# Optimization experiments

Measured on AMD Instinct MI355X. Metric: run time of the kernel, lower is better.

## Reference

```python
import jax, jax.numpy as jnp
import numpy as np

B, N, D, H = 4, 8192, 1024, 16
C = D // H  # head dim = 64
EPS = 1e-6


def setup_inputs() -> dict:
    key = jax.random.key(0)
    ks = jax.random.split(key, 8)
    sc = 0.02
    return {
        "q": jax.random.normal(ks[0], (B, N, D), jnp.float32),
        "k": jax.random.normal(ks[1], (B, N, D), jnp.float32),
        "v": jax.random.normal(ks[2], (B, N, D), jnp.float32),
        "Wq": jax.random.normal(ks[3], (D, D), jnp.float32) * sc,
        "Wk": jax.random.normal(ks[4], (D, D), jnp.float32) * sc,
        "Wv": jax.random.normal(ks[5], (D, D), jnp.float32) * sc,
        "Wproj": jax.random.normal(ks[6], (D, D), jnp.float32) * sc,
        "focusing_factor": jnp.asarray(3.0, jnp.float32),
    }


def _to_heads(x):
    # b n (h c) -> (b h) n c
    return x.reshape(B, N, H, C).transpose(0, 2, 1, 3).reshape(B * H, N, C)


def reference(q, k, v, Wq, Wk, Wv, Wproj, focusing_factor):
    # projections (torch Linear: x @ W.T, no bias)
    qp = q @ Wq.T
    kp = k @ Wk.T
    vp = v @ Wv.T

    def feature_map(x):
        # |GELU(x)| + eps, then focused renormalization:
        # softmax(focusing_factor * log(f)) * mean(f)
        f = jnp.abs(jax.nn.gelu(x, approximate=False)) + EPS
        f_norm = f.mean(axis=-1, keepdims=True)
        return jax.nn.softmax(jnp.log(f) * focusing_factor, axis=-1) * f_norm

    qf = feature_map(qp)
    kf = feature_map(kp)

    qh = _to_heads(qf)  # [B*H, N, C]
    kh = _to_heads(kf)
    vh = _to_heads(vp)

    k_mean = kh.mean(axis=1)  # [B*H, C]
    z_inv = jnp.einsum('bnd,bd->bn', qh, k_mean) + EPS  # [B*H, N]

    # (k/sqrt(N))^T (v/sqrt(N)) == (k^T v)/N
    kv = jnp.einsum('bnc,bnd->bcd', kh, vh) / N  # [B*H, C, C]
    y = jnp.einsum('bic,bcd->bid', qh, kv) / z_inv[..., None]  # [B*H, N, C]

    y = y.reshape(B, H, N, C).transpose(0, 2, 1, 3).reshape(B, N, D)
    return y @ Wproj.T
```

## Files before the change

### kernel.cpp

```cpp
#include <hip/hip_runtime.h>

using f16 = _Float16;
typedef __attribute__((ext_vector_type(4))) _Float16 f16x4;
typedef __attribute__((ext_vector_type(8))) _Float16 f16x8;
typedef __attribute__((ext_vector_type(4))) float f32x4;

#define DEVI __device__ __forceinline__

namespace {

constexpr int BB = 4;
constexpr int NN = 8192;
constexpr int DD = 1024;
constexpr int MTOT = BB * NN;
constexpr float FSCALE = 64.0f;
constexpr float ZCONST = 64.0f * 64.0f * (8192.0f * 1e-6f);

DEVI void gl16(const void* g, void* l) {
  __builtin_amdgcn_global_load_lds(
      (__attribute__((address_space(1))) void*)(void*)g,
      (__attribute__((address_space(3))) void*)l, 16, 0, 0);
}

DEVI float wsum(float v) {
#pragma unroll
  for (int m = 32; m > 0; m >>= 1) v += __shfl_xor(v, m, 64);
  return v;
}
DEVI float wmaxr(float v) {
#pragma unroll
  for (int m = 32; m > 0; m >>= 1) v = fmaxf(v, __shfl_xor(v, m, 64));
  return v;
}
DEVI float block_sum(float v, float* sred, int tid) {
  v = wsum(v);
  __syncthreads();
  if ((tid & 63) == 0) sred[tid >> 6] = v;
  __syncthreads();
  return sred[0] + sred[1] + sred[2] + sred[3];
}
DEVI float block_max(float v, float* sred, int tid) {
  v = wmaxr(v);
  __syncthreads();
  if ((tid & 63) == 0) sred[tid >> 6] = v;
  __syncthreads();
  return fmaxf(fmaxf(sred[0], sred[1]), fmaxf(sred[2], sred[3]));
}

struct CastArgs {
  const float* src[8];
  f16* dst[8];
  int n4[8];
};

__global__ __launch_bounds__(256) void cast_kernel(CastArgs a) {
  const int z = blockIdx.y;
  const float4* __restrict__ s = (const float4*)a.src[z];
  f16x4* __restrict__ d = (f16x4*)a.dst[z];
  const int n4 = a.n4[z];
  for (int i = blockIdx.x * blockDim.x + threadIdx.x; i < n4;
       i += gridDim.x * blockDim.x) {
    float4 f = s[i];
    f16x4 o = {(f16)f.x, (f16)f.y, (f16)f.z, (f16)f.w};
    d[i] = o;
  }
}

struct Gemm3 {
  const f16* A[3];
  const f16* Bt[3];
  void* C[3];
};
struct Gemm3f {
  const float* A[3];
  const f16* Bt[3];
  f16* C[3];
};

#define GEMM_PREAMBLE()                                                      \
  constexpr int K = DD;                                                      \
  constexpr int N = DD;                                                      \
  constexpr int NKT = K / 64;                                                \
  const int nx = gridDim.x;                                                  \
  int lin = blockIdx.y * nx + blockIdx.x;                                    \
  const int cpx = (gridDim.y * nx) >> 3;                                     \
  lin = (lin & 7) * cpx + (lin >> 3);                                        \
  const size_t row0 = (size_t)(lin / nx) * 256;                              \
  const size_t col0 = (size_t)(lin % nx) * 256;                              \
  const int tid = threadIdx.x, lane = tid & 63, wv = tid >> 6;               \
  const int wm = wv >> 2, wn = wv & 3;                                       \
  const int fr = lane & 15, f7 = lane & 7, kq = lane >> 4;                   \
  const int srow = wv * 8 + (lane >> 3);                                     \
  const int ssw = (lane & 7) ^ ((lane >> 3) & 7);                            \
  const int c0e = (kq ^ f7) * 8;

__global__ __launch_bounds__(512, 2) void gemm256_fa(Gemm3f P) {
  GEMM_PREAMBLE()
  const int z = blockIdx.z;
  const float* __restrict__ A = P.A[z];
  const f16* __restrict__ Bt = P.Bt[z];
  f16* __restrict__ C = P.C[z];

  __shared__ __align__(16) f16 LA[2][2][8192];
  __shared__ __align__(16) f16 LB[2][2][8192];

  auto stageB = [&](int kts, int half) {
    const f16* src = Bt + (col0 + half * 128 + srow) * K + kts * 64 + ssw * 8;
    f16* dst = &LB[kts & 1][half][wv * 512];
#pragma unroll
    for (int c = 0; c < 2; ++c) gl16(src + (size_t)c * 64 * K, dst + c * 4096);
  };

  const int ar = tid >> 2;
  const int ac2 = (tid & 3) * 2;
  auto loadA = [&](int kts, float4* r) {
#pragma unroll
    for (int half = 0; half < 2; ++half) {
      const float* src = A + (row0 + half * 128 + ar) * (size_t)K + kts * 64;
#pragma unroll
      for (int c = 0; c < 2; ++c) {
        r[half * 4 + 2 * c + 0] = *(const float4*)(src + (ac2 + c) * 8);
        r[half * 4 + 2 * c + 1] = *(const float4*)(src + (ac2 + c) * 8 + 4);
      }
    }
  };
  auto writeA = [&](int kts, const float4* r) {
#pragma unroll
    for (int half = 0; half < 2; ++half) {
      f16* base = &LA[kts & 1][half][ar * 64];
#pragma unroll
      for (int c = 0; c < 2; ++c) {
        const float4 lo = r[half * 4 + 2 * c], hi = r[half * 4 + 2 * c + 1];
        f16x8 o = {(f16)lo.x, (f16)lo.y, (f16)lo.z, (f16)lo.w,
                   (f16)hi.x, (f16)hi.y, (f16)hi.z, (f16)hi.w};
        *(f16x8*)&base[((ac2 + c) ^ (ar & 7)) * 8] = o;
      }
    }
  };

  f32x4 acc[8][4];
#pragma unroll
  for (int i = 0; i < 8; ++i)
#pragma unroll
    for (int j = 0; j < 4; ++j) acc[i][j] = f32x4{0.f, 0.f, 0.f, 0.f};

  float4 ra[8];
  loadA(0, ra);
  stageB(0, 0); stageB(0, 1);
  asm volatile("s_waitcnt vmcnt(0)" ::: "memory");
  writeA(0, ra);
  asm volatile("s_waitcnt lgkmcnt(0)" ::: "memory");
  loadA(1, ra);
  __builtin_amdgcn_s_barrier();

  for (int kt = 0; kt < NKT; ++kt) {
    const int buf = kt & 1;
    const f16* Ah = LA[buf][wm];
    const f16* Bh = &LB[buf][wn >> 1][(wn & 1) * 4096];
    f16x8 a0[8], a1[8], b0[4], b1[4];

#pragma unroll
    for (int mi = 0; mi < 8; ++mi)
      a0[mi] = *(const f16x8*)&Ah[(mi * 16 + fr) * 64 + c0e];
#pragma unroll
    for (int ni = 0; ni < 4; ++ni)
      b0[ni] = *(const f16x8*)&Bh[(ni * 16 + fr) * 64 + c0e];
    if (kt + 1 < NKT) stageB(kt + 1, 0);
    __builtin_amdgcn_s_barrier();
    asm volatile("s_waitcnt lgkmcnt(0)" ::: "memory");
    __builtin_amdgcn_sched_barrier(0);
    __builtin_amdgcn_s_setprio(1);
#pragma unroll
    for (int mi = 0; mi < 4; ++mi)
#pragma unroll
      for (int ni = 0; ni < 4; ++ni)
        acc[mi][ni] = __builtin_amdgcn_mfma_f32_16x16x32_f16(
            a0[mi], b0[ni], acc[mi][ni], 0, 0, 0);
    __builtin_amdgcn_s_setprio(0);
    __builtin_amdgcn_s_barrier();

#pragma unroll
    for (int mi = 0; mi < 8; ++mi)
      a1[mi] = *(const f16x8*)&Ah[(mi * 16 + fr) * 64 + (c0e ^ 32)];
    if (kt + 1 < NKT) stageB(kt + 1, 1);
    __builtin_amdgcn_s_barrier();
    asm volatile("s_waitcnt lgkmcnt(0)" ::: "memory");
    __builtin_amdgcn_sched_barrier(0);
    __builtin_amdgcn_s_setprio(1);
#pragma unroll
    for (int mi = 4; mi < 8; ++mi)
#pragma unroll
      for (int ni = 0; ni < 4; ++ni)
        acc[mi][ni] = __builtin_amdgcn_mfma_f32_16x16x32_f16(
            a0[mi], b0[ni], acc[mi][ni], 0, 0, 0);
    __builtin_amdgcn_s_setprio(0);
    __builtin_amdgcn_s_barrier();

#pragma unroll
    for (int ni = 0; ni < 4; ++ni)
      b1[ni] = *(const f16x8*)&Bh[(ni * 16 + fr) * 64 + (c0e ^ 32)];
    __builtin_amdgcn_s_barrier();
    asm volatile("s_waitcnt lgkmcnt(0)" ::: "memory");
    __builtin_amdgcn_sched_barrier(0);
    __builtin_amdgcn_s_setprio(1);
#pragma unroll
    for (int mi = 0; mi < 4; ++mi)
#pragma unroll
      for (int ni = 0; ni < 4; ++ni)
        acc[mi][ni] = __builtin_amdgcn_mfma_f32_16x16x32_f16(
            a1[mi], b1[ni], acc[mi][ni], 0, 0, 0);
    __builtin_amdgcn_s_setprio(0);
    __builtin_amdgcn_s_barrier();

    __builtin_amdgcn_s_setprio(1);
#pragma unroll
    for (int mi = 4; mi < 8; ++mi)
#pragma unroll
      for (int ni = 0; ni < 4; ++ni)
        acc[mi][ni] = __builtin_amdgcn_mfma_f32_16x16x32_f16(
            a1[mi], b1[ni], acc[mi][ni], 0, 0, 0);
    __builtin_amdgcn_s_setprio(0);
    asm volatile("s_waitcnt vmcnt(0)" ::: "memory");
    __builtin_amdgcn_sched_barrier(0);
    if (kt + 1 < NKT) {
      writeA(kt + 1, ra);
      asm volatile("s_waitcnt lgkmcnt(0)" ::: "memory");
      if (kt + 2 < NKT) loadA(kt + 2, ra);
    }
    __builtin_amdgcn_s_barrier();
  }

#pragma unroll
  for (int mi = 0; mi < 8; ++mi)
#pragma unroll
    for (int ni = 0; ni < 4; ++ni) {
      const size_t colv = col0 + wn * 64 + ni * 16 + fr;
#pragma unroll
      for (int r = 0; r < 4; ++r) {
        const size_t rowv = row0 + wm * 128 + mi * 16 + (lane >> 4) * 4 + r;
        C[rowv * N + colv] = (f16)acc[mi][ni][r];
      }
    }
}

template <typename OutT>
__global__ __launch_bounds__(512, 2) void gemm256(Gemm3 P) {
  GEMM_PREAMBLE()
  const int z = blockIdx.z;
  const f16* __restrict__ A = P.A[z];
  const f16* __restrict__ Bt = P.Bt[z];
  OutT* __restrict__ C = (OutT*)P.C[z];

  __shared__ __align__(16) f16 LA[2][2][8192];
  __shared__ __align__(16) f16 LB[2][2][8192];

  auto stageA = [&](int kts, int half) {
    const f16* src = A + (row0 + half * 128 + srow) * K + kts * 64 + ssw * 8;
    f16* dst = &LA[kts & 1][half][wv * 512];
#pragma unroll
    for (int c = 0; c < 2; ++c) gl16(src + (size_t)c * 64 * K, dst + c * 4096);
  };
  auto stageB = [&](int kts, int half) {
    const f16* src = Bt + (col0 + half * 128 + srow) * K + kts * 64 + ssw * 8;
    f16* dst = &LB[kts & 1][half][wv * 512];
#pragma unroll
    for (int c = 0; c < 2; ++c) gl16(src + (size_t)c * 64 * K, dst + c * 4096);
  };

  f32x4 acc[8][4];
#pragma unroll
  for (int i = 0; i < 8; ++i)
#pragma unroll
    for (int j = 0; j < 4; ++j) acc[i][j] = f32x4{0.f, 0.f, 0.f, 0.f};

  stageA(0, 0); stageA(0, 1); stageB(0, 0); stageB(0, 1);
  stageA(1, 0); stageA(1, 1);
  asm volatile("s_waitcnt vmcnt(4)" ::: "memory");
  __builtin_amdgcn_s_barrier();

  for (int kt = 0; kt < NKT; ++kt) {
    const int buf = kt & 1;
    const f16* Ah = LA[buf][wm];
    const f16* Bh = &LB[buf][wn >> 1][(wn & 1) * 4096];
    f16x8 a0[8], a1[8], b0[4], b1[4];

#pragma unroll
    for (int mi = 0; mi < 8; ++mi)
      a0[mi] = *(const f16x8*)&Ah[(mi * 16 + fr) * 64 + c0e];
#pragma unroll
    for (int ni = 0; ni < 4; ++ni)
      b0[ni] = *(const f16x8*)&Bh[(ni * 16 + fr) * 64 + c0e];
    if (kt < NKT - 1) stageB(kt + 1, 0);
    __builtin_amdgcn_s_barrier();
    asm volatile("s_waitcnt lgkmcnt(0)" ::: "memory");
    __builtin_amdgcn_sched_barrier(0);
    __builtin_amdgcn_s_setprio(1);
#pragma unroll
    for (int mi = 0; mi < 4; ++mi)
#pragma unroll
      for (int ni = 0; ni < 4; ++ni)
        acc[mi][ni] = __builtin_amdgcn_mfma_f32_16x16x32_f16(
            a0[mi], b0[ni], acc[mi][ni], 0, 0, 0);
    __builtin_amdgcn_s_setprio(0);
    __builtin_amdgcn_s_barrier();

#pragma unroll
    for (int mi = 0; mi < 8; ++mi)
      a1[mi] = *(const f16x8*)&Ah[(mi * 16 + fr) * 64 + (c0e ^ 32)];
    if (kt < NKT - 1) stageB(kt + 1, 1);
    __builtin_amdgcn_s_barrier();
    asm volatile("s_waitcnt lgkmcnt(0)" ::: "memory");
    __builtin_amdgcn_sched_barrier(0);
    __builtin_amdgcn_s_setprio(1);
#pragma unroll
    for (int mi = 4; mi < 8; ++mi)
#pragma unroll
      for (int ni = 0; ni < 4; ++ni)
        acc[mi][ni] = __builtin_amdgcn_mfma_f32_16x16x32_f16(
            a0[mi], b0[ni], acc[mi][ni], 0, 0, 0);
    __builtin_amdgcn_s_setprio(0);
    __builtin_amdgcn_s_barrier();

#pragma unroll
    for (int ni = 0; ni < 4; ++ni)
      b1[ni] = *(const f16x8*)&Bh[(ni * 16 + fr) * 64 + (c0e ^ 32)];
    if (kt < NKT - 2) stageA(kt + 2, 0);
    __builtin_amdgcn_s_barrier();
    asm volatile("s_waitcnt lgkmcnt(0)" ::: "memory");
    __builtin_amdgcn_sched_barrier(0);
    __builtin_amdgcn_s_setprio(1);
#pragma unroll
    for (int mi = 0; mi < 4; ++mi)
#pragma unroll
      for (int ni = 0; ni < 4; ++ni)
        acc[mi][ni] = __builtin_amdgcn_mfma_f32_16x16x32_f16(
            a1[mi], b1[ni], acc[mi][ni], 0, 0, 0);
    __builtin_amdgcn_s_setprio(0);
    __builtin_amdgcn_s_barrier();

    if (kt < NKT - 2) stageA(kt + 2, 1);
    __builtin_amdgcn_s_barrier();
    __builtin_amdgcn_s_setprio(1);
#pragma unroll
    for (int mi = 4; mi < 8; ++mi)
#pragma unroll
      for (int ni = 0; ni < 4; ++ni)
        acc[mi][ni] = __builtin_amdgcn_mfma_f32_16x16x32_f16(
            a1[mi], b1[ni], acc[mi][ni], 0, 0, 0);
    __builtin_amdgcn_s_setprio(0);
    if (kt < NKT - 2)
      asm volatile("s_waitcnt vmcnt(4)" ::: "memory");
    else
      asm volatile("s_waitcnt vmcnt(0)" ::: "memory");
    __builtin_amdgcn_s_barrier();
  }

#pragma unroll
  for (int mi = 0; mi < 8; ++mi)
#pragma unroll
    for (int ni = 0; ni < 4; ++ni) {
      const size_t colv = col0 + wn * 64 + ni * 16 + fr;
#pragma unroll
      for (int r = 0; r < 4; ++r) {
        const size_t rowv = row0 + wm * 128 + mi * 16 + (lane >> 4) * 4 + r;
        C[rowv * N + colv] = (OutT)acc[mi][ni][r];
      }
    }
}

__global__ __launch_bounds__(256) void feature_kernel(
    const f16* __restrict__ qp, const f16* __restrict__ kp,
    f16* __restrict__ qf, f16* __restrict__ kf, const float* __restrict__ ffp) {
  const int row = blockIdx.x;
  const int tid = threadIdx.x;
  const bool isq = (blockIdx.y == 0);
  const f16* __restrict__ src = isq ? qp : kp;
  f16* __restrict__ dst = isq ? qf : kf;
  const float ff = ffp[0];
  __shared__ float sred[4];

  f16x4 xv = ((const f16x4*)src)[(size_t)row * 256 + tid];
  float f0[4];
  float ps = 0.f;
#pragma unroll
  for (int j = 0; j < 4; ++j) {
    float x = (float)xv[j];
    float g = 0.5f * x * (1.0f + erff(x * 0.70710678118654752f));
    float fv = fabsf(g) + 1e-6f;
    f0[j] = fv;
    ps += fv;
  }
  float fsum = block_sum(ps, sred, tid);
  float t[4];
  float pm = -1e30f;
#pragma unroll
  for (int j = 0; j < 4; ++j) {
    t[j] = ff * __logf(f0[j]);
    pm = fmaxf(pm, t[j]);
  }
  float tmax = block_max(pm, sred, tid);
  float e[4];
  float es = 0.f;
#pragma unroll
  for (int j = 0; j < 4; ++j) {
    e[j] = __expf(t[j] - tmax);
    es += e[j];
  }
  float esum = block_sum(es, sred, tid);
  const float scale = fsum * (1.0f / 1024.0f) / esum * FSCALE;
  f16x4 o;
#pragma unroll
  for (int j = 0; j < 4; ++j) o[j] = (f16)(e[j] * scale);
  ((f16x4*)dst)[(size_t)row * 256 + tid] = o;
}

__global__ __launch_bounds__(256) void kv_kernel(
    const f16* __restrict__ kf, const f16* __restrict__ vp,
    float* __restrict__ kvsum, float* __restrict__ colsum) {
  const int bh = blockIdx.x;
  const int b = bh >> 4, h = bh & 15;
  const int tid = threadIdx.x, lane = tid & 63, wave = tid >> 6;
  __shared__ __align__(16) f16 kt[32 * 64];
  __shared__ __align__(16) f16 vt[32 * 64];
  __shared__ float csred[4][64];

  f32x4 acc[4];
#pragma unroll
  for (int ni = 0; ni < 4; ++ni) acc[ni] = f32x4{0.f, 0.f, 0.f, 0.f};
  float cpart = 0.f;

  const int srow = wave * 8 + (lane >> 3);
  const int scol = (lane & 7) * 8;
  const int colbase = h * 64;
  const int n0base = blockIdx.y * 512;

  for (int n0 = n0base; n0 < n0base + 512; n0 += 32) {
    const size_t gofs = ((size_t)(b * NN + n0 + srow)) * DD + colbase + scol;
    gl16(kf + gofs, &kt[wave * 512]);
    gl16(vp + gofs, &vt[wave * 512]);
    __syncthreads();
    {
      const int c = tid & 63;
      const int r0 = (tid >> 6) * 8;
#pragma unroll
      for (int rr = 0; rr < 8; ++rr) cpart += (float)kt[(r0 + rr) * 64 + c];
    }
    f16x8 a, bfr[4];
#pragma unroll
    for (int j = 0; j < 8; ++j)
      a[j] = kt[((lane >> 4) * 8 + j) * 64 + wave * 16 + (lane & 15)];
#pragma unroll
    for (int ni = 0; ni < 4; ++ni)
#pragma unroll
      for (int j = 0; j < 8; ++j)
        bfr[ni][j] = vt[((lane >> 4) * 8 + j) * 64 + ni * 16 + (lane & 15)];
#pragma unroll
    for (int ni = 0; ni < 4; ++ni)
      acc[ni] = __builtin_amdgcn_mfma_f32_16x16x32_f16(a, bfr[ni], acc[ni], 0, 0, 0);
    __syncthreads();
  }
#pragma unroll
  for (int ni = 0; ni < 4; ++ni)
#pragma unroll
    for (int r = 0; r < 4; ++r) {
      const int c = wave * 16 + (lane >> 4) * 4 + r;
      const int d = ni * 16 + (lane & 15);
      atomicAdd(&kvsum[(size_t)bh * 4096 + c * 64 + d], acc[ni][r]);
    }
  csred[tid >> 6][tid & 63] = cpart;
  __syncthreads();
  if (tid < 64)
    atomicAdd(&colsum[bh * 64 + tid],
              csred[0][tid] + csred[1][tid] + csred[2][tid] + csred[3][tid]);
}

__global__ __launch_bounds__(256) void y_kernel(
    const f16* __restrict__ qf, const f16* __restrict__ kv16,
    const float* __restrict__ colsum, f16* __restrict__ y) {
  const int bh = blockIdx.x, b = bh >> 4, h = bh & 15;
  const int n0 = blockIdx.y * 128;
  const int tid = threadIdx.x, lane = tid & 63, wave = tid >> 6;
  __shared__ __align__(16) f16 qs[128 * 64];
  __shared__ __align__(16) f16 kvs[64 * 64];
  __shared__ float cs[64];
  __shared__ float zr[128];

#pragma unroll
  for (int cc = 0; cc < 4; ++cc) {
    const int r = wave * 32 + cc * 8 + (lane >> 3);
    gl16(qf + ((size_t)(b * NN + n0 + r)) * DD + h * 64 + (lane & 7) * 8,
         &qs[(wave * 4 + cc) * 512]);
  }
#pragma unroll
  for (int cc = 0; cc < 2; ++cc) {
    const int r = wave * 16 + cc * 8 + (lane >> 3);
    gl16(kv16 + (size_t)bh * 4096 + r * 64 + (lane & 7) * 8,
         &kvs[(wave * 2 + cc) * 512]);
  }
  if (tid < 64) cs[tid] = colsum[bh * 64 + tid];
  __syncthreads();
  if (tid < 128) {
    float zv = 0.f;
    for (int cc = 0; cc < 64; ++cc) {
      const int c = (cc + tid) & 63;
      zv += (float)qs[tid * 64 + c] * cs[c];
    }
    zr[tid] = zv + ZCONST;
  }
  __syncthreads();

  f32x4 acc[2][4];
#pragma unroll
  for (int mi = 0; mi < 2; ++mi)
#pragma unroll
    for (int ni = 0; ni < 4; ++ni) acc[mi][ni] = f32x4{0.f, 0.f, 0.f, 0.f};

#pragma unroll
  for (int ks = 0; ks < 2; ++ks) {
    f16x8 a[2], bfr[4];
#pragma unroll
    for (int mi = 0; mi < 2; ++mi)
      a[mi] = *(const f16x8*)&qs[(wave * 32 + mi * 16 + (lane & 15)) * 64 +
                                 ks * 32 + (lane >> 4) * 8];
#pragma unroll
    for (int ni = 0; ni < 4; ++ni)
#pragma unroll
      for (int j = 0; j < 8; ++j)
        bfr[ni][j] = kvs[(ks * 32 + (lane >> 4) * 8 + j) * 64 + ni * 16 + (lane & 15)];
#pragma unroll
    for (int mi = 0; mi < 2; ++mi)
#pragma unroll
      for (int ni = 0; ni < 4; ++ni)
        acc[mi][ni] = __builtin_amdgcn_mfma_f32_16x16x32_f16(
            a[mi], bfr[ni], acc[mi][ni], 0, 0, 0);
  }
#pragma unroll
  for (int mi = 0; mi < 2; ++mi)
#pragma unroll
    for (int ni = 0; ni < 4; ++ni)
#pragma unroll
      for (int r = 0; r < 4; ++r) {
        const int rrow = wave * 32 + mi * 16 + (lane >> 4) * 4 + r;
        const int d = ni * 16 + (lane & 15);
        const float yv = acc[mi][ni][r] / zr[rrow];
        y[((size_t)(b * NN + n0 + rrow)) * DD + h * 64 + d] = (f16)yv;
      }
}

}

extern "C" void kernel_launch(void* const* d_in, const int* in_sizes, int n_in,
                              void* d_out, int out_size, void* d_ws, size_t ws_size,
                              hipStream_t stream) {
  const float* q = (const float*)d_in[0];
  const float* k = (const float*)d_in[1];
  const float* v = (const float*)d_in[2];
  const float* Wq = (const float*)d_in[3];
  const float* Wk = (const float*)d_in[4];
  const float* Wv = (const float*)d_in[5];
  const float* Wp = (const float*)d_in[6];
  const float* ffp = (const float*)d_in[7];

  char* w = (char*)d_ws;
  size_t off = 0;
  auto alloc = [&](size_t b) {
    void* p = (void*)(w + off);
    off += (b + 255) & ~(size_t)255;
    return p;
  };
  const size_t big = (size_t)MTOT * DD * sizeof(f16);
  f16* qp16 = (f16*)alloc(big);
  f16* kp16 = (f16*)alloc(big);
  f16* vp16 = (f16*)alloc(big);
  f16* qf  = (f16*)alloc(big);
  f16* kf  = (f16*)alloc(big);
  f16* y16 = (f16*)alloc(big);
  f16* Wq16 = (f16*)alloc((size_t)DD * DD * 2);
  f16* Wk16 = (f16*)alloc((size_t)DD * DD * 2);
  f16* Wv16 = (f16*)alloc((size_t)DD * DD * 2);
  f16* Wp16 = (f16*)alloc((size_t)DD * DD * 2);
  float* kvsum = (float*)alloc(64 * 64 * 64 * sizeof(float));
  float* colsum = (float*)alloc(64 * 64 * sizeof(float));
  f16* kv16 = (f16*)alloc(64 * 64 * 64 * sizeof(f16));
  if (off > ws_size) return;

  CastArgs ca{};
  ca.src[0] = Wq; ca.dst[0] = Wq16; ca.n4[0] = DD * DD / 4;
  ca.src[1] = Wk; ca.dst[1] = Wk16; ca.n4[1] = DD * DD / 4;
  ca.src[2] = Wv; ca.dst[2] = Wv16; ca.n4[2] = DD * DD / 4;
  ca.src[3] = Wp; ca.dst[3] = Wp16; ca.n4[3] = DD * DD / 4;
  cast_kernel<<<dim3(128, 4), 256, 0, stream>>>(ca);

  Gemm3f gp{};
  gp.A[0] = q; gp.Bt[0] = Wq16; gp.C[0] = qp16;
  gp.A[1] = k; gp.Bt[1] = Wk16; gp.C[1] = kp16;
  gp.A[2] = v; gp.Bt[2] = Wv16; gp.C[2] = vp16;
  gemm256_fa<<<dim3(DD / 256, MTOT / 256, 3), 512, 0, stream>>>(gp);

  feature_kernel<<<dim3(MTOT, 2), 256, 0, stream>>>(qp16, kp16, qf, kf, ffp);

  hipMemsetAsync(kvsum, 0, 64 * 64 * 64 * sizeof(float) + 64 * 64 * sizeof(float),
                 stream);
  kv_kernel<<<dim3(64, 16), 256, 0, stream>>>(kf, vp16, kvsum, colsum);

  CastArgs cb{};
  cb.src[0] = kvsum; cb.dst[0] = kv16; cb.n4[0] = 64 * 64 * 64 / 4;
  cast_kernel<<<dim3(64, 1), 256, 0, stream>>>(cb);

  y_kernel<<<dim3(64, 64), 256, 0, stream>>>(qf, kv16, colsum, y16);

  Gemm3 gf{};
  gf.A[0] = y16; gf.Bt[0] = Wp16; gf.C[0] = d_out;
  gemm256<float><<<dim3(DD / 256, MTOT / 256, 1), 512, 0, stream>>>(gf);
}
```

Before: 598.0 us.

## Use one wave per row in feature kernel, drop max pass, approximate erf

The feature map kernel now gives each 1024-wide row to a single 64-lane wave, with each lane handling 16 values loaded as two 8-wide f16 vectors. This removes the block-level shared-memory reductions and barriers. The softmax max-subtraction pass is dropped, and erff is replaced by the Abramowitz–Stegun polynomial approximation built on __expf. The aim is to cut synchronisation and transcendental cost in a memory-bound elementwise kernel. The trade-off is a small accuracy loss in GELU, plus a risk of exp overflow in f32 if the focusing factor makes ff*log(f) large.

```diff
diff --git a/kernel.cpp b/kernel.cpp
--- a/kernel.cpp
+++ b/kernel.cpp
@@ -26,25 +26,6 @@
 #pragma unroll
   for (int m = 32; m > 0; m >>= 1) v += __shfl_xor(v, m, 64);
   return v;
-}
-DEVI float wmaxr(float v) {
-#pragma unroll
-  for (int m = 32; m > 0; m >>= 1) v = fmaxf(v, __shfl_xor(v, m, 64));
-  return v;
-}
-DEVI float block_sum(float v, float* sred, int tid) {
-  v = wsum(v);
-  __syncthreads();
-  if ((tid & 63) == 0) sred[tid >> 6] = v;
-  __syncthreads();
-  return sred[0] + sred[1] + sred[2] + sred[3];
-}
-DEVI float block_max(float v, float* sred, int tid) {
-  v = wmaxr(v);
-  __syncthreads();
-  if ((tid & 63) == 0) sred[tid >> 6] = v;
-  __syncthreads();
-  return fmaxf(fmaxf(sred[0], sred[1]), fmaxf(sred[2], sred[3]));
 }
 
 struct CastArgs {
@@ -371,47 +352,55 @@
 __global__ __launch_bounds__(256) void feature_kernel(
     const f16* __restrict__ qp, const f16* __restrict__ kp,
     f16* __restrict__ qf, f16* __restrict__ kf, const float* __restrict__ ffp) {
-  const int row = blockIdx.x;
-  const int tid = threadIdx.x;
+  const int lane = threadIdx.x & 63;
+  const size_t row = (size_t)blockIdx.x * 4 + (threadIdx.x >> 6);
   const bool isq = (blockIdx.y == 0);
   const f16* __restrict__ src = isq ? qp : kp;
   f16* __restrict__ dst = isq ? qf : kf;
   const float ff = ffp[0];
-  __shared__ float sred[4];
-
-  f16x4 xv = ((const f16x4*)src)[(size_t)row * 256 + tid];
-  float f0[4];
+
+  const f16x8* p = (const f16x8*)(src + row * DD + lane * 16);
+  f16x8 v0 = p[0], v1 = p[1];
+
+  float f0[16];
   float ps = 0.f;
 #pragma unroll
-  for (int j = 0; j < 4; ++j) {
-    float x = (float)xv[j];
-    float g = 0.5f * x * (1.0f + erff(x * 0.70710678118654752f));
-    float fv = fabsf(g) + 1e-6f;
+  for (int j = 0; j < 16; ++j) {
+    const float x = (float)(j < 8 ? v0[j] : v1[j - 8]);
+    const float ax = fabsf(x) * 0.70710678118654752f;
+    const float tt = 1.0f / (1.0f + 0.3275911f * ax);
+    const float poly =
+        tt * (0.254829592f +
+              tt * (-0.284496736f +
+                    tt * (1.421413741f +
+                          tt * (-1.453152027f + tt * 1.061405429f))));
+    const float erfv = 1.0f - poly * __expf(-ax * ax);
+    const float g = 0.5f * x * (1.0f + copysignf(erfv, x));
+    const float fv = fabsf(g) + 1e-6f;
     f0[j] = fv;
     ps += fv;
   }
-  float fsum = block_sum(ps, sred, tid);
-  float t[4];
-  float pm = -1e30f;
-#pragma unroll
-  for (int j = 0; j < 4; ++j) {
-    t[j] = ff * __logf(f0[j]);
-    pm = fmaxf(pm, t[j]);
-  }
-  float tmax = block_max(pm, sred, tid);
-  float e[4];
+  const float fsum = wsum(ps);
+
+  float e[16];
   float es = 0.f;
 #pragma unroll
-  for (int j = 0; j < 4; ++j) {
-    e[j] = __expf(t[j] - tmax);
+  for (int j = 0; j < 16; ++j) {
+    e[j] = __expf(ff * __logf(f0[j]));
     es += e[j];
   }
-  float esum = block_sum(es, sred, tid);
+  const float esum = wsum(es);
+
   const float scale = fsum * (1.0f / 1024.0f) / esum * FSCALE;
-  f16x4 o;
-#pragma unroll
-  for (int j = 0; j < 4; ++j) o[j] = (f16)(e[j] * scale);
-  ((f16x4*)dst)[(size_t)row * 256 + tid] = o;
+  f16x8 o0, o1;
+#pragma unroll
+  for (int j = 0; j < 8; ++j) {
+    o0[j] = (f16)(e[j] * scale);
+    o1[j] = (f16)(e[j + 8] * scale);
+  }
+  f16x8* q = (f16x8*)(dst + row * DD + lane * 16);
+  q[0] = o0;
+  q[1] = o1;
 }
 
 __global__ __launch_bounds__(256) void kv_kernel(
@@ -597,7 +586,7 @@
   gp.A[2] = v; gp.Bt[2] = Wv16; gp.C[2] = vp16;
   gemm256_fa<<<dim3(DD / 256, MTOT / 256, 3), 512, 0, stream>>>(gp);
 
-  feature_kernel<<<dim3(MTOT, 2), 256, 0, stream>>>(qp16, kp16, qf, kf, ffp);
+  feature_kernel<<<dim3(MTOT / 4, 2), 256, 0, stream>>>(qp16, kp16, qf, kf, ffp);
 
   hipMemsetAsync(kvsum, 0, 64 * 64 * 64 * sizeof(float) + 64 * 64 * sizeof(float),
                  stream);
```

After: 585.7 us. 2.1% less time.
